# Kernel optimization log

Measured on AMD Instinct MI355X. Metric: run time of the kernel, lower is better.

## Reference

```python
import jax, jax.numpy as jnp
import numpy as np


def setup_inputs() -> dict:
    key = jax.random.key(0)
    k1, k2, kq, kk, kv = jax.random.split(key, 5)
    D = 1024
    N1 = 4096
    N2 = 4096
    s = 1.0 / np.sqrt(D)  # ~ PyTorch Linear init scale
    return {
        "x1": jax.random.normal(k1, (N1, D), dtype=jnp.float32),
        "x2": jax.random.normal(k2, (N2, D), dtype=jnp.float32),
        "Wq": jax.random.uniform(kq, (D, D), dtype=jnp.float32, minval=-s, maxval=s),
        "Wk": jax.random.uniform(kk, (D, D), dtype=jnp.float32, minval=-s, maxval=s),
        "Wv": jax.random.uniform(kv, (D, D), dtype=jnp.float32, minval=-s, maxval=s),
    }


def reference(x1, x2, Wq, Wk, Wv):
    # Linear(input_dim, input_dim, bias=False): y = x @ W^T
    Q = x1 @ Wq.T          # [N1, D]
    K = x2 @ Wk.T          # [N2, D]
    V = x2 @ Wv.T          # [N2, D]
    scores = Q @ K.T       # [N1, N2]  (no 1/sqrt(d) scaling in original)
    weights = jax.nn.softmax(scores, axis=-1)
    return weights @ V     # [N1, D]
```

## Files before the change

kernel.cpp:

```cpp
#include <hip/hip_runtime.h>
#include <cstdint>
#include <cstddef>

typedef _Float16 f16x8 __attribute__((ext_vector_type(8)));
typedef _Float16 f16x4 __attribute__((ext_vector_type(4)));
typedef float f32x4 __attribute__((ext_vector_type(4)));

__device__ __forceinline__ void gload_lds16(const _Float16* g, void* l) {
  __builtin_amdgcn_global_load_lds(
      (const __attribute__((address_space(1))) void*)(g),
      (__attribute__((address_space(3))) void*)(l), 16, 0, 0);
}

struct GDesc {
  const _Float16* A;
  const _Float16* B;
  void* C;
  int lda, ldb, ldc, nbm, nbn;
};

template <typename CT, bool MULTI>
__global__ __launch_bounds__(512, 2) void gemmq(
    GDesc d0, GDesc d1, GDesc d2,
    int inner, int nKT, int ksOff, size_t cSplit) {
  __shared__ __align__(16) char smem[131072];

  const int bid = blockIdx.x;
  const int gi  = bid / inner;
  int ib        = bid % inner;

  GDesc d = d0;
  if (MULTI) { if (gi == 1) d = d1; else if (gi == 2) d = d2; }
  const _Float16* A = d.A;
  const _Float16* B = d.B;
  CT* C = (CT*)d.C;
  if (!MULTI) {
    A += (size_t)gi * ksOff;
    B += (size_t)gi * ksOff;
    C += (size_t)gi * cSplit;
  }
  const int lda = d.lda, ldb = d.ldb, ldc = d.ldc, nbn = d.nbn;

  ib = (ib & 7) * (inner >> 3) + (ib >> 3);
  const int brow = (ib / nbn) << 8;
  const int bcol = (ib % nbn) << 8;

  const int tid = threadIdx.x;
  const int w   = tid >> 6;
  const int l   = tid & 63;
  const int wm  = w >> 2;
  const int wn  = w & 3;

  const int sRow = l >> 2;
  const int sCol = (((l & 3) ^ ((l >> 3) & 3)) << 3);
  const _Float16* gA0 = A + (size_t)(brow + (w << 4) + sRow) * lda + sCol;
  const _Float16* gA1 = A + (size_t)(brow + ((w + 8) << 4) + sRow) * lda + sCol;
  const _Float16* gB0 = B + (size_t)(bcol + (w << 4) + sRow) * ldb + sCol;
  const _Float16* gB1 = B + (size_t)(bcol + ((w + 8) << 4) + sRow) * ldb + sCol;

  const int axr = (l >> 1) & 3;
  const int fq  = ((l >> 4) ^ axr) << 4;
  const int aBase = (wm << 13) + ((l & 15) << 6) + fq;
  const int bBase = (wn << 12) + ((l & 15) << 6) + fq;

  f32x4 acc[8][4] = {};

#pragma unroll
  for (int t = 0; t < 3; ++t) {
    char* Ab = smem + t * 32768;
    char* Bb = Ab + 16384;
    gload_lds16(gA0 + t * 32, Ab + (w << 10));
    gload_lds16(gA1 + t * 32, Ab + ((w + 8) << 10));
    gload_lds16(gB0 + t * 32, Bb + (w << 10));
    gload_lds16(gB1 + t * 32, Bb + ((w + 8) << 10));
  }
  asm volatile("s_waitcnt vmcnt(8)" ::: "memory");
  __builtin_amdgcn_s_barrier();
  __builtin_amdgcn_sched_barrier(0);

  for (int j = 0; j < nKT; ++j) {
    const char* Ab = smem + (j & 3) * 32768;
    const char* Bb = Ab + 16384;
    const int jn = j + 3;
    char* AbN = smem + (jn & 3) * 32768;
    char* BbN = AbN + 16384;
    const bool st = (jn < nKT);

    if (st) {
      gload_lds16(gA0 + jn * 32, AbN + (w << 10));
      gload_lds16(gA1 + jn * 32, AbN + ((w + 8) << 10));
    }
    f16x8 bf[4], af[4];
#pragma unroll
    for (int n = 0; n < 4; ++n)
      bf[n] = *(const f16x8*)(Bb + bBase + (n << 10));
#pragma unroll
    for (int m = 0; m < 4; ++m)
      af[m] = *(const f16x8*)(Ab + aBase + (m << 10));
    __builtin_amdgcn_s_barrier();
    __builtin_amdgcn_s_setprio(1);
#pragma unroll
    for (int m = 0; m < 4; ++m)
#pragma unroll
      for (int n = 0; n < 4; ++n)
        acc[m][n] = __builtin_amdgcn_mfma_f32_16x16x32_f16(af[m], bf[n], acc[m][n], 0, 0, 0);
    __builtin_amdgcn_s_setprio(0);
    __builtin_amdgcn_s_barrier();
    __builtin_amdgcn_sched_barrier(0);

    if (st) {
      gload_lds16(gB0 + jn * 32, BbN + (w << 10));
      gload_lds16(gB1 + jn * 32, BbN + ((w + 8) << 10));
    }
#pragma unroll
    for (int m = 0; m < 4; ++m)
      af[m] = *(const f16x8*)(Ab + aBase + ((m + 4) << 10));
    __builtin_amdgcn_s_barrier();
    __builtin_amdgcn_s_setprio(1);
#pragma unroll
    for (int m = 0; m < 4; ++m)
#pragma unroll
      for (int n = 0; n < 4; ++n)
        acc[m + 4][n] = __builtin_amdgcn_mfma_f32_16x16x32_f16(af[m], bf[n], acc[m + 4][n], 0, 0, 0);
    __builtin_amdgcn_s_setprio(0);
    asm volatile("s_waitcnt vmcnt(8)" ::: "memory");
    __builtin_amdgcn_s_barrier();
    __builtin_amdgcn_sched_barrier(0);
  }
  asm volatile("s_waitcnt vmcnt(0)" ::: "memory");

  const int crow0 = brow + (wm << 7) + ((l >> 4) << 2);
  const int ccol  = bcol + (wn << 6) + (l & 15);
#pragma unroll
  for (int m = 0; m < 8; ++m)
#pragma unroll
    for (int n = 0; n < 4; ++n)
#pragma unroll
      for (int jj = 0; jj < 4; ++jj)
        C[(size_t)(crow0 + (m << 4) + jj) * ldc + ccol + (n << 4)] = (CT)acc[m][n][jj];
}

__global__ __launch_bounds__(256) void softmax_rows(const float* __restrict__ S,
                                                    _Float16* __restrict__ P,
                                                    int N) {
  __shared__ float buf[4096];
  __shared__ float red[8];
  const int row = blockIdx.x;
  const int tid = threadIdx.x;
  const int n4  = N >> 2;
  const float4* s4 = (const float4*)(S + (size_t)row * N);
  float4* b4 = (float4*)buf;

  float m = -3.4e38f;
  for (int i = tid; i < n4; i += 256) {
    float4 v = s4[i];
    b4[i] = v;
    m = fmaxf(m, fmaxf(fmaxf(v.x, v.y), fmaxf(v.z, v.w)));
  }
  for (int off = 32; off > 0; off >>= 1) m = fmaxf(m, __shfl_xor(m, off));
  if ((tid & 63) == 0) red[tid >> 6] = m;
  __syncthreads();
  m = fmaxf(fmaxf(red[0], red[1]), fmaxf(red[2], red[3]));

  float sum = 0.f;
  for (int i = tid; i < n4; i += 256) {
    float4 v = b4[i];
    v.x = __expf(v.x - m); v.y = __expf(v.y - m);
    v.z = __expf(v.z - m); v.w = __expf(v.w - m);
    b4[i] = v;
    sum += (v.x + v.y) + (v.z + v.w);
  }
  for (int off = 32; off > 0; off >>= 1) sum += __shfl_xor(sum, off);
  if ((tid & 63) == 0) red[4 + (tid >> 6)] = sum;
  __syncthreads();
  sum = (red[4] + red[5]) + (red[6] + red[7]);
  const float inv = 1.f / sum;

  f16x4* p4 = (f16x4*)(P + (size_t)row * N);
  for (int i = tid; i < n4; i += 256) {
    float4 v = b4[i];
    f16x4 h = { (_Float16)(v.x * inv), (_Float16)(v.y * inv),
                (_Float16)(v.z * inv), (_Float16)(v.w * inv) };
    p4[i] = h;
  }
}

__global__ __launch_bounds__(256) void cast_f32_f16(const float* __restrict__ in,
                                                    _Float16* __restrict__ out, int n4) {
  int i = blockIdx.x * 256 + threadIdx.x;
  if (i < n4) {
    float4 v = ((const float4*)in)[i];
    f16x4 h = { (_Float16)v.x, (_Float16)v.y, (_Float16)v.z, (_Float16)v.w };
    ((f16x4*)out)[i] = h;
  }
}

__global__ __launch_bounds__(256) void reduce4(const float* __restrict__ p,
                                               float* __restrict__ out,
                                               int n4, size_t stride4) {
  int i = blockIdx.x * 256 + threadIdx.x;
  if (i >= n4) return;
  const float4* p4 = (const float4*)p;
  float4 a = p4[i];
  float4 b = p4[i + stride4];
  float4 c = p4[i + 2 * stride4];
  float4 d = p4[i + 3 * stride4];
  float4 r = { (a.x + b.x) + (c.x + d.x), (a.y + b.y) + (c.y + d.y),
               (a.z + b.z) + (c.z + d.z), (a.w + b.w) + (c.w + d.w) };
  ((float4*)out)[i] = r;
}

extern "C" void kernel_launch(void* const* d_in, const int* in_sizes, int n_in,
                              void* d_out, int out_size, void* d_ws, size_t ws_size,
                              hipStream_t stream) {
  const int D  = 1024;
  const int N1 = in_sizes[0] / D;
  const int N2 = in_sizes[1] / D;

  const float* x1 = (const float*)d_in[0];
  const float* x2 = (const float*)d_in[1];
  const float* Wq = (const float*)d_in[2];
  const float* Wk = (const float*)d_in[3];
  const float* Wv = (const float*)d_in[4];
  float* out = (float*)d_out;

  _Float16* x1h = (_Float16*)d_ws;
  _Float16* x2h = x1h + (size_t)N1 * D;
  _Float16* Wqh = x2h + (size_t)N2 * D;
  _Float16* Wkh = Wqh + (size_t)D * D;
  _Float16* Wvh = Wkh + (size_t)D * D;
  _Float16* Qh  = Wvh + (size_t)D * D;
  _Float16* Kh  = Qh  + (size_t)N1 * D;
  _Float16* Vt  = Kh  + (size_t)N2 * D;
  _Float16* P   = Vt  + (size_t)D * N2;
  float*    S   = (float*)(P + (size_t)N1 * N2);

  auto cast = [&](const float* src, _Float16* dst, size_t n) {
    int n4 = (int)(n >> 2);
    cast_f32_f16<<<dim3((n4 + 255) / 256), 256, 0, stream>>>(src, dst, n4);
  };
  cast(x1, x1h, (size_t)N1 * D);
  cast(x2, x2h, (size_t)N2 * D);
  cast(Wq, Wqh, (size_t)D * D);
  cast(Wk, Wkh, (size_t)D * D);
  cast(Wv, Wvh, (size_t)D * D);

  {
    GDesc dq = { x1h, Wqh, Qh, D, D, D, N1 / 256, D / 256 };
    GDesc dk = { x2h, Wkh, Kh, D, D, D, N2 / 256, D / 256 };
    GDesc dv = { Wvh, x2h, Vt, D, D, N2, D / 256, N2 / 256 };
    gemmq<_Float16, true><<<dim3(192), 512, 0, stream>>>(dq, dk, dv, 64, D / 32, 0, 0);
  }
  {
    GDesc dsd = { Qh, Kh, S, D, D, N2, N1 / 256, N2 / 256 };
    gemmq<float, false><<<dim3(256), 512, 0, stream>>>(dsd, dsd, dsd, 256, D / 32, 0, 0);
  }
  softmax_rows<<<dim3(N1), 256, 0, stream>>>(S, P, N2);
  {
    GDesc dp = { P, Vt, S, N2, N2, D, N1 / 256, D / 256 };
    gemmq<float, false><<<dim3(256), 512, 0, stream>>>(dp, dp, dp, 64, 1024 / 32, 1024,
                                                       (size_t)N1 * D);
  }
  reduce4<<<dim3((N1 * D / 4 + 255) / 256), 256, 0, stream>>>(
      S, out, N1 * D / 4, (size_t)N1 * D / 4);
}
```

Baseline: 167.1 us.

## Software-pipeline GEMM fragments through registers with one barrier per K tile

```diff
diff --git a/kernel.cpp b/kernel.cpp
--- a/kernel.cpp
+++ b/kernel.cpp
@@ -18,6 +18,58 @@
   void* C;
   int lda, ldb, ldc, nbm, nbn;
 };
+
+struct SetA { f16x8 b[4]; f16x8 a[4]; };
+struct SetB { f16x8 a[4]; };
+
+__device__ __forceinline__ void tile_body(
+    int t, int nKT, SetA& cur, SetA& nxt, SetB& sbv, char* smem,
+    const _Float16* gA0, const _Float16* gA1,
+    const _Float16* gB0, const _Float16* gB1,
+    int w, int aBase, int bBase, f32x4 (&acc)[8][4]) {
+  asm volatile("s_waitcnt vmcnt(4)" ::: "memory");
+  __builtin_amdgcn_s_barrier();
+  const int jc = (t + 3 < nKT) ? t + 3 : nKT - 1;
+  char* dst = smem + (jc & 3) * 32768;
+  gload_lds16(gA0 + jc * 32, dst + (w << 10));
+  gload_lds16(gA1 + jc * 32, dst + ((w + 8) << 10));
+  gload_lds16(gB0 + jc * 32, dst + 16384 + (w << 10));
+  gload_lds16(gB1 + jc * 32, dst + 16384 + ((w + 8) << 10));
+
+  const char* Ab = smem + (t & 3) * 32768;
+#pragma unroll
+  for (int m = 0; m < 4; ++m)
+    sbv.a[m] = *(const f16x8*)(Ab + aBase + ((m + 4) << 10));
+  asm volatile("s_waitcnt lgkmcnt(4)" ::: "memory");
+  __builtin_amdgcn_sched_barrier(0);
+
+  const char* AbN = smem + ((t + 1) & 3) * 32768;
+  const char* BbN = AbN + 16384;
+#pragma unroll
+  for (int n = 0; n < 4; ++n)
+    nxt.b[n] = *(const f16x8*)(BbN + bBase + (n << 10));
+#pragma unroll
+  for (int m = 0; m < 4; ++m)
+    nxt.a[m] = *(const f16x8*)(AbN + aBase + (m << 10));
+  __builtin_amdgcn_sched_barrier(0);
+
+  __builtin_amdgcn_s_setprio(1);
+#pragma unroll
+  for (int m = 0; m < 4; ++m)
+#pragma unroll
+    for (int n = 0; n < 4; ++n)
+      acc[m][n] = __builtin_amdgcn_mfma_f32_16x16x32_f16(cur.a[m], cur.b[n], acc[m][n], 0, 0, 0);
+  __builtin_amdgcn_s_setprio(0);
+  asm volatile("s_waitcnt lgkmcnt(8)" ::: "memory");
+  __builtin_amdgcn_sched_barrier(0);
+  __builtin_amdgcn_s_setprio(1);
+#pragma unroll
+  for (int m = 0; m < 4; ++m)
+#pragma unroll
+    for (int n = 0; n < 4; ++n)
+      acc[m + 4][n] = __builtin_amdgcn_mfma_f32_16x16x32_f16(sbv.a[m], cur.b[n], acc[m + 4][n], 0, 0, 0);
+  __builtin_amdgcn_s_setprio(0);
+}
 
 template <typename CT, bool MULTI>
 __global__ __launch_bounds__(512, 2) void gemmq(
@@ -64,70 +116,33 @@
   const int bBase = (wn << 12) + ((l & 15) << 6) + fq;
 
   f32x4 acc[8][4] = {};
-
-#pragma unroll
-  for (int t = 0; t < 3; ++t) {
-    char* Ab = smem + t * 32768;
-    char* Bb = Ab + 16384;
-    gload_lds16(gA0 + t * 32, Ab + (w << 10));
-    gload_lds16(gA1 + t * 32, Ab + ((w + 8) << 10));
-    gload_lds16(gB0 + t * 32, Bb + (w << 10));
-    gload_lds16(gB1 + t * 32, Bb + ((w + 8) << 10));
+  SetA s0, s1;
+  SetB sbv;
+
+#pragma unroll
+  for (int tt = 0; tt < 3; ++tt) {
+    char* dst = smem + tt * 32768;
+    gload_lds16(gA0 + tt * 32, dst + (w << 10));
+    gload_lds16(gA1 + tt * 32, dst + ((w + 8) << 10));
+    gload_lds16(gB0 + tt * 32, dst + 16384 + (w << 10));
+    gload_lds16(gB1 + tt * 32, dst + 16384 + ((w + 8) << 10));
   }
   asm volatile("s_waitcnt vmcnt(8)" ::: "memory");
   __builtin_amdgcn_s_barrier();
-  __builtin_amdgcn_sched_barrier(0);
-
-  for (int j = 0; j < nKT; ++j) {
-    const char* Ab = smem + (j & 3) * 32768;
-    const char* Bb = Ab + 16384;
-    const int jn = j + 3;
-    char* AbN = smem + (jn & 3) * 32768;
-    char* BbN = AbN + 16384;
-    const bool st = (jn < nKT);
-
-    if (st) {
-      gload_lds16(gA0 + jn * 32, AbN + (w << 10));
-      gload_lds16(gA1 + jn * 32, AbN + ((w + 8) << 10));
-    }
-    f16x8 bf[4], af[4];
-#pragma unroll
-    for (int n = 0; n < 4; ++n)
-      bf[n] = *(const f16x8*)(Bb + bBase + (n << 10));
-#pragma unroll
-    for (int m = 0; m < 4; ++m)
-      af[m] = *(const f16x8*)(Ab + aBase + (m << 10));
-    __builtin_amdgcn_s_barrier();
-    __builtin_amdgcn_s_setprio(1);
-#pragma unroll
-    for (int m = 0; m < 4; ++m)
-#pragma unroll
-      for (int n = 0; n < 4; ++n)
-        acc[m][n] = __builtin_amdgcn_mfma_f32_16x16x32_f16(af[m], bf[n], acc[m][n], 0, 0, 0);
-    __builtin_amdgcn_s_setprio(0);
-    __builtin_amdgcn_s_barrier();
-    __builtin_amdgcn_sched_barrier(0);
-
-    if (st) {
-      gload_lds16(gB0 + jn * 32, BbN + (w << 10));
-      gload_lds16(gB1 + jn * 32, BbN + ((w + 8) << 10));
-    }
-#pragma unroll
-    for (int m = 0; m < 4; ++m)
-      af[m] = *(const f16x8*)(Ab + aBase + ((m + 4) << 10));
-    __builtin_amdgcn_s_barrier();
-    __builtin_amdgcn_s_setprio(1);
-#pragma unroll
-    for (int m = 0; m < 4; ++m)
-#pragma unroll
-      for (int n = 0; n < 4; ++n)
-        acc[m + 4][n] = __builtin_amdgcn_mfma_f32_16x16x32_f16(af[m], bf[n], acc[m + 4][n], 0, 0, 0);
-    __builtin_amdgcn_s_setprio(0);
-    asm volatile("s_waitcnt vmcnt(8)" ::: "memory");
-    __builtin_amdgcn_s_barrier();
-    __builtin_amdgcn_sched_barrier(0);
-  }
-  asm volatile("s_waitcnt vmcnt(0)" ::: "memory");
+  {
+    const char* Ab = smem;
+    const char* Bb = smem + 16384;
+#pragma unroll
+    for (int n = 0; n < 4; ++n) s0.b[n] = *(const f16x8*)(Bb + bBase + (n << 10));
+#pragma unroll
+    for (int m = 0; m < 4; ++m) s0.a[m] = *(const f16x8*)(Ab + aBase + (m << 10));
+  }
+
+  for (int t = 0; t < nKT; t += 2) {
+    tile_body(t,     nKT, s0, s1, sbv, smem, gA0, gA1, gB0, gB1, w, aBase, bBase, acc);
+    tile_body(t + 1, nKT, s1, s0, sbv, smem, gA0, gA1, gB0, gB1, w, aBase, bBase, acc);
+  }
+  asm volatile("s_waitcnt vmcnt(0) lgkmcnt(0)" ::: "memory");
 
   const int crow0 = brow + (wm << 7) + ((l >> 4) << 2);
   const int ccol  = bcol + (wn << 6) + (l & 15);
```

New measurement: 162.4 us. 2.8% less time.

## Restructure GEMM main loop to double-buffered 64-wide K tiles

Applied to the files above, without the earlier changes.

```diff
diff --git a/kernel.cpp b/kernel.cpp
--- a/kernel.cpp
+++ b/kernel.cpp
@@ -18,6 +18,9 @@
   void* C;
   int lda, ldb, ldc, nbm, nbn;
 };
+
+#define MFMA16(d, va, vb) \
+  d = __builtin_amdgcn_mfma_f32_16x16x32_f16(va, vb, d, 0, 0, 0)
 
 template <typename CT, bool MULTI>
 __global__ __launch_bounds__(512, 2) void gemmq(
@@ -65,69 +68,95 @@
 
   f32x4 acc[8][4] = {};
 
-#pragma unroll
-  for (int t = 0; t < 3; ++t) {
-    char* Ab = smem + t * 32768;
-    char* Bb = Ab + 16384;
-    gload_lds16(gA0 + t * 32, Ab + (w << 10));
-    gload_lds16(gA1 + t * 32, Ab + ((w + 8) << 10));
-    gload_lds16(gB0 + t * 32, Bb + (w << 10));
-    gload_lds16(gB1 + t * 32, Bb + ((w + 8) << 10));
-  }
-  asm volatile("s_waitcnt vmcnt(8)" ::: "memory");
+  {
+    char* nb = smem;
+    gload_lds16(gA0 + 0,  nb + (w << 10));
+    gload_lds16(gA1 + 0,  nb + ((w + 8) << 10));
+    gload_lds16(gB0 + 0,  nb + 32768 + (w << 10));
+    gload_lds16(gB1 + 0,  nb + 32768 + ((w + 8) << 10));
+    gload_lds16(gA0 + 32, nb + 16384 + (w << 10));
+    gload_lds16(gA1 + 32, nb + 16384 + ((w + 8) << 10));
+    gload_lds16(gB0 + 32, nb + 49152 + (w << 10));
+    gload_lds16(gB1 + 32, nb + 49152 + ((w + 8) << 10));
+  }
+  asm volatile("s_waitcnt vmcnt(4)" ::: "memory");
   __builtin_amdgcn_s_barrier();
-  __builtin_amdgcn_sched_barrier(0);
-
-  for (int j = 0; j < nKT; ++j) {
-    const char* Ab = smem + (j & 3) * 32768;
-    const char* Bb = Ab + 16384;
-    const int jn = j + 3;
-    char* AbN = smem + (jn & 3) * 32768;
-    char* BbN = AbN + 16384;
-    const bool st = (jn < nKT);
-
-    if (st) {
-      gload_lds16(gA0 + jn * 32, AbN + (w << 10));
-      gload_lds16(gA1 + jn * 32, AbN + ((w + 8) << 10));
-    }
-    f16x8 bf[4], af[4];
-#pragma unroll
-    for (int n = 0; n < 4; ++n)
-      bf[n] = *(const f16x8*)(Bb + bBase + (n << 10));
-#pragma unroll
-    for (int m = 0; m < 4; ++m)
-      af[m] = *(const f16x8*)(Ab + aBase + (m << 10));
-    __builtin_amdgcn_s_barrier();
-    __builtin_amdgcn_s_setprio(1);
-#pragma unroll
-    for (int m = 0; m < 4; ++m)
-#pragma unroll
-      for (int n = 0; n < 4; ++n)
-        acc[m][n] = __builtin_amdgcn_mfma_f32_16x16x32_f16(af[m], bf[n], acc[m][n], 0, 0, 0);
-    __builtin_amdgcn_s_setprio(0);
-    __builtin_amdgcn_s_barrier();
-    __builtin_amdgcn_sched_barrier(0);
-
-    if (st) {
-      gload_lds16(gB0 + jn * 32, BbN + (w << 10));
-      gload_lds16(gB1 + jn * 32, BbN + ((w + 8) << 10));
-    }
-#pragma unroll
-    for (int m = 0; m < 4; ++m)
-      af[m] = *(const f16x8*)(Ab + aBase + ((m + 4) << 10));
-    __builtin_amdgcn_s_barrier();
-    __builtin_amdgcn_s_setprio(1);
-#pragma unroll
-    for (int m = 0; m < 4; ++m)
-#pragma unroll
-      for (int n = 0; n < 4; ++n)
-        acc[m + 4][n] = __builtin_amdgcn_mfma_f32_16x16x32_f16(af[m], bf[n], acc[m + 4][n], 0, 0, 0);
-    __builtin_amdgcn_s_setprio(0);
-    asm volatile("s_waitcnt vmcnt(8)" ::: "memory");
-    __builtin_amdgcn_s_barrier();
-    __builtin_amdgcn_sched_barrier(0);
-  }
-  asm volatile("s_waitcnt vmcnt(0)" ::: "memory");
+
+  for (int t = 0; t < nKT; ++t) {
+    const char* cb = smem + (t & 1) * 65536;
+    char* nb = smem + ((t + 1) & 1) * 65536;
+    const int jc = (t + 1 < nKT) ? t + 1 : nKT - 1;
+    const int kof = jc * 64;
+
+    f16x8 bf[4], a0f[4], a4f[4];
+
+#pragma unroll
+    for (int n = 0; n < 4; ++n) bf[n]  = *(const f16x8*)(cb + 32768 + bBase + (n << 10));
+#pragma unroll
+    for (int m = 0; m < 4; ++m) a0f[m] = *(const f16x8*)(cb + aBase + (m << 10));
+    gload_lds16(gA0 + kof, nb + (w << 10));
+    gload_lds16(gA1 + kof, nb + ((w + 8) << 10));
+    __builtin_amdgcn_s_barrier();
+    asm volatile("s_waitcnt lgkmcnt(0)" ::: "memory");
+    __builtin_amdgcn_sched_barrier(0);
+    __builtin_amdgcn_s_setprio(1);
+#pragma unroll
+    for (int m = 0; m < 4; ++m)
+#pragma unroll
+      for (int n = 0; n < 4; ++n) MFMA16(acc[m][n], a0f[m], bf[n]);
+    __builtin_amdgcn_s_setprio(0);
+    __builtin_amdgcn_s_barrier();
+
+#pragma unroll
+    for (int m = 0; m < 4; ++m) a4f[m] = *(const f16x8*)(cb + aBase + ((m + 4) << 10));
+    gload_lds16(gB0 + kof, nb + 32768 + (w << 10));
+    gload_lds16(gB1 + kof, nb + 32768 + ((w + 8) << 10));
+    __builtin_amdgcn_s_barrier();
+    asm volatile("s_waitcnt lgkmcnt(0)" ::: "memory");
+    __builtin_amdgcn_sched_barrier(0);
+    __builtin_amdgcn_s_setprio(1);
+#pragma unroll
+    for (int m = 0; m < 4; ++m)
+#pragma unroll
+      for (int n = 0; n < 4; ++n) MFMA16(acc[m + 4][n], a4f[m], bf[n]);
+    __builtin_amdgcn_s_setprio(0);
+    asm volatile("s_waitcnt vmcnt(4)" ::: "memory");
+    __builtin_amdgcn_s_barrier();
+
+#pragma unroll
+    for (int n = 0; n < 4; ++n) bf[n]  = *(const f16x8*)(cb + 49152 + bBase + (n << 10));
+#pragma unroll
+    for (int m = 0; m < 4; ++m) a0f[m] = *(const f16x8*)(cb + 16384 + aBase + (m << 10));
+    gload_lds16(gA0 + kof + 32, nb + 16384 + (w << 10));
+    gload_lds16(gA1 + kof + 32, nb + 16384 + ((w + 8) << 10));
+    __builtin_amdgcn_s_barrier();
+    asm volatile("s_waitcnt lgkmcnt(0)" ::: "memory");
+    __builtin_amdgcn_sched_barrier(0);
+    __builtin_amdgcn_s_setprio(1);
+#pragma unroll
+    for (int m = 0; m < 4; ++m)
+#pragma unroll
+      for (int n = 0; n < 4; ++n) MFMA16(acc[m][n], a0f[m], bf[n]);
+    __builtin_amdgcn_s_setprio(0);
+    __builtin_amdgcn_s_barrier();
+
+#pragma unroll
+    for (int m = 0; m < 4; ++m) a4f[m] = *(const f16x8*)(cb + 16384 + aBase + ((m + 4) << 10));
+    gload_lds16(gB0 + kof + 32, nb + 49152 + (w << 10));
+    gload_lds16(gB1 + kof + 32, nb + 49152 + ((w + 8) << 10));
+    __builtin_amdgcn_s_barrier();
+    asm volatile("s_waitcnt lgkmcnt(0)" ::: "memory");
+    __builtin_amdgcn_sched_barrier(0);
+    __builtin_amdgcn_s_setprio(1);
+#pragma unroll
+    for (int m = 0; m < 4; ++m)
+#pragma unroll
+      for (int n = 0; n < 4; ++n) MFMA16(acc[m + 4][n], a4f[m], bf[n]);
+    __builtin_amdgcn_s_setprio(0);
+    asm volatile("s_waitcnt vmcnt(4)" ::: "memory");
+    __builtin_amdgcn_s_barrier();
+  }
+  asm volatile("s_waitcnt vmcnt(0) lgkmcnt(0)" ::: "memory");
 
   const int crow0 = brow + (wm << 7) + ((l >> 4) << 2);
   const int ccol  = bcol + (wn << 6) + (l & 15);
@@ -249,16 +278,16 @@
     GDesc dq = { x1h, Wqh, Qh, D, D, D, N1 / 256, D / 256 };
     GDesc dk = { x2h, Wkh, Kh, D, D, D, N2 / 256, D / 256 };
     GDesc dv = { Wvh, x2h, Vt, D, D, N2, D / 256, N2 / 256 };
-    gemmq<_Float16, true><<<dim3(192), 512, 0, stream>>>(dq, dk, dv, 64, D / 32, 0, 0);
+    gemmq<_Float16, true><<<dim3(192), 512, 0, stream>>>(dq, dk, dv, 64, D / 64, 0, 0);
   }
   {
     GDesc dsd = { Qh, Kh, S, D, D, N2, N1 / 256, N2 / 256 };
-    gemmq<float, false><<<dim3(256), 512, 0, stream>>>(dsd, dsd, dsd, 256, D / 32, 0, 0);
+    gemmq<float, false><<<dim3(256), 512, 0, stream>>>(dsd, dsd, dsd, 256, D / 64, 0, 0);
   }
   softmax_rows<<<dim3(N1), 256, 0, stream>>>(S, P, N2);
   {
     GDesc dp = { P, Vt, S, N2, N2, D, N1 / 256, D / 256 };
-    gemmq<float, false><<<dim3(256), 512, 0, stream>>>(dp, dp, dp, 64, 1024 / 32, 1024,
+    gemmq<float, false><<<dim3(256), 512, 0, stream>>>(dp, dp, dp, 64, 1024 / 64, 1024,
                                                        (size_t)N1 * D);
   }
   reduce4<<<dim3((N1 * D / 4 + 255) / 256), 256, 0, stream>>>(
```

After: 163.4 us. 1.02x faster.
